# Kernel optimization log

Measured on AMD Instinct MI355X. Metric: run time of the kernel, lower is better.

Reference implementation:

```python
import jax, jax.numpy as jnp
import numpy as np
from jax import lax

THRESHOLD = 1.0
TAU_M = 10.0
TAU_S = 5.0
T_REF = 2.0


def setup_inputs() -> dict:
    key = jax.random.key(0)
    k1, k2, k3, k4 = jax.random.split(key, 4)
    T, B, I, O = 256, 128, 1024, 512
    x = (jax.random.uniform(k1, (T, B, I)) < 0.2).astype(jnp.float32)
    weight = jax.random.normal(k2, (O, I), dtype=jnp.float32) * 0.05
    bias = jax.random.normal(k3, (O,), dtype=jnp.float32) * 0.01
    weight_lateral = jax.random.normal(k4, (O,), dtype=jnp.float32) * 0.01
    return {"x": x, "weight": weight, "bias": bias, "weight_lateral": weight_lateral}


def reference(x, weight, bias, weight_lateral):
    # x: [T, B, I]; weight: [O, I]; bias, weight_lateral: [O]
    T, B, I = x.shape
    O = weight.shape[0]
    f32 = x.dtype
    decay_s = jnp.asarray(1.0 - 1.0 / TAU_S, f32)
    decay_m = jnp.asarray(1.0 - 1.0 / TAU_M, f32)

    def step(carry, xt):
        ep, u, o, v_ref, t_pre, t_post, t = carry
        # per-step linear + lateral feedback of previous output spikes
        i_resp = xt @ weight.T + bias + o * weight_lateral  # [B, O]
        ep = ep * decay_s + i_resp
        u = u * decay_m + ep / TAU_S
        u = u * (1.0 - (v_ref > 0).astype(f32))        # refractory gating
        o = (u > THRESHOLD).astype(f32)                # spike
        v_ref = jnp.clip(T_REF * o + (v_ref - 1.0), 0.0, T_REF)
        t_pre = jnp.maximum(xt * (t + 1.0) - 1.0, t_pre)   # last pre-spike time
        t_post = jnp.maximum(o * (t + 1.0) - 1.0, t_post)  # last post-spike time
        return (ep, u, o, v_ref, t_pre, t_post, t + 1.0), o

    zBO = jnp.zeros((B, O), f32)
    init = (zBO, zBO, zBO, zBO,
            jnp.full((B, I), -1.0, f32),
            jnp.full((B, O), -1.0, f32),
            jnp.asarray(0.0, f32))
    carry, output = lax.scan(step, init, x)
    times_pre, times_post = carry[4], carry[5]
    return output, times_pre, times_post
```

## Files before the change

kernel.cpp:

```cpp
#include <hip/hip_runtime.h>

#define T_STEPS 256
#define B_SZ 128
#define I_SZ 1024
#define O_SZ 512

typedef short bf16x8 __attribute__((ext_vector_type(8)));
typedef float f32x16 __attribute__((ext_vector_type(16)));

#define PLANE (O_SZ * I_SZ)
#define WS_NEEDED ((size_t)3 * PLANE * 2)

__device__ __forceinline__ ushort f2bf_rne(float f) {
    uint u = __float_as_uint(f);
    u += ((u >> 16) & 1u) + 0x7fffu;
    return (ushort)(u >> 16);
}
__device__ __forceinline__ uint pk2(float lo, float hi) {
    return (__float_as_uint(lo) >> 16) | (__float_as_uint(hi) & 0xffff0000u);
}
__device__ __forceinline__ void gload_lds16(const void* g, void* l) {
    typedef const void __attribute__((address_space(1))) gvt;
    typedef void __attribute__((address_space(3))) svt;
    __builtin_amdgcn_global_load_lds((gvt*)g, (svt*)l, 16, 0, 0);
}

__global__ __launch_bounds__(256) void wsplit_kernel(
    const float* __restrict__ W, ushort* __restrict__ wsp)
{
    const int t = blockIdx.x * 256 + threadIdx.x;
    const int n = t >> 7, kq = t & 127, k0 = kq * 8;
    const float* wp = W + (size_t)n * I_SZ + k0;

    uint q1[4], q2[4], q3[4];
#pragma unroll
    for (int jj = 0; jj < 4; ++jj) {
        ushort s1[2], s2[2], s3[2];
#pragma unroll
        for (int e = 0; e < 2; ++e) {
            float w0 = wp[jj * 2 + e];
            ushort a1 = f2bf_rne(w0);
            float  f1 = __uint_as_float((uint)a1 << 16);
            float  r1 = w0 - f1;
            ushort a2 = f2bf_rne(r1);
            float  f2 = __uint_as_float((uint)a2 << 16);
            float  r2 = r1 - f2;
            ushort a3 = f2bf_rne(r2);
            s1[e] = a1; s2[e] = a2; s3[e] = a3;
        }
        q1[jj] = (uint)s1[0] | ((uint)s1[1] << 16);
        q2[jj] = (uint)s2[0] | ((uint)s2[1] << 16);
        q3[jj] = (uint)s3[0] | ((uint)s3[1] << 16);
    }
    const int kt = k0 >> 5, k16 = (k0 >> 4) & 1, kh = (k0 >> 3) & 1;
    const int l = (n & 31) | (kh << 5), nsg = n >> 5;
    const size_t off = ((((size_t)kt * 16 + nsg) * 2 + k16) * 64 + l) * 8;
    *(uint4*)(wsp + off)             = make_uint4(q1[0], q1[1], q1[2], q1[3]);
    *(uint4*)(wsp + PLANE + off)     = make_uint4(q2[0], q2[1], q2[2], q2[3]);
    *(uint4*)(wsp + 2 * PLANE + off) = make_uint4(q3[0], q3[1], q3[2], q3[3]);
}

__global__ __launch_bounds__(512, 2) void gemm_mfma4(
    const float* __restrict__ X, const ushort* __restrict__ wsp,
    const float* __restrict__ bias, float* __restrict__ S)
{
    __shared__ uint ldsA[8192];
    __shared__ uint ldsB[24576];

    const int tid  = threadIdx.x;
    const int lane = tid & 63;
    const int w    = tid >> 6;
    const int wm   = w >> 2, wn = w & 3;

    const int bid     = blockIdx.x;
    const int logical = (bid & 7) * 32 + (bid >> 3);
    const int mb = logical >> 1, nb = logical & 1;
    const int row0 = mb * 256;

    const int arow = w * 32 + (lane >> 3);
    const int akq  = lane & 7;
    const float* pa = X + (size_t)(row0 + arow) * I_SZ + akq * 4;
    uint adst[4];
#pragma unroll
    for (int i = 0; i < 4; ++i) {
        const int row = arow + i * 8;
        adst[i] = (((row >> 5) * 2 + (akq >> 2)) * 64 +
                   ((row & 31) | (((akq >> 1) & 1) << 5))) * 4 + (akq & 1) * 2;
    }

    uint bsrc[6];
    const int c0 = w * 6;
#pragma unroll
    for (int i = 0; i < 6; ++i) {
        const int c = c0 + i, p = c >> 4, rr = (c >> 1) & 7, k16 = c & 1;
        bsrc[i] = (uint)p * PLANE + (uint)(((nb * 8 + rr) * 2 + k16) * 512) + lane * 8;
    }

    f32x16 acc[4][2];
#pragma unroll
    for (int i = 0; i < 4; ++i)
#pragma unroll
        for (int j = 0; j < 2; ++j)
#pragma unroll
            for (int r = 0; r < 16; ++r) acc[i][j][r] = 0.f;

#define BFRAG(BASE, P, SN, SS) \
    (*(const bf16x8*)((BASE) + (((P) * 8 + wn * 2 + (SN)) * 2 + (SS)) * 256 + lane * 4))

#define CLUSTER(B00, B01, B10, B11) do {                                      \
    __builtin_amdgcn_s_setprio(1);                                            \
    _Pragma("unroll")                                                         \
    for (int m_ = 0; m_ < 4; ++m_) {                                          \
        acc[m_][0] = __builtin_amdgcn_mfma_f32_32x32x16_bf16(af[m_][0], B00, acc[m_][0], 0, 0, 0); \
        acc[m_][0] = __builtin_amdgcn_mfma_f32_32x32x16_bf16(af[m_][1], B01, acc[m_][0], 0, 0, 0); \
        acc[m_][1] = __builtin_amdgcn_mfma_f32_32x32x16_bf16(af[m_][0], B10, acc[m_][1], 0, 0, 0); \
        acc[m_][1] = __builtin_amdgcn_mfma_f32_32x32x16_bf16(af[m_][1], B11, acc[m_][1], 0, 0, 0); \
    }                                                                         \
    __builtin_amdgcn_s_setprio(0);                                            \
} while (0)

    {
#pragma unroll
        for (int i = 0; i < 6; ++i)
            gload_lds16(wsp + bsrc[i], ldsB + (c0 + i) * 256);
        float4 a0 = *(const float4*)(pa);
        float4 a1 = *(const float4*)(pa + 8 * I_SZ);
        float4 a2 = *(const float4*)(pa + 16 * I_SZ);
        float4 a3 = *(const float4*)(pa + 24 * I_SZ);
        *(uint2*)(ldsA + adst[0]) = make_uint2(pk2(a0.x, a0.y), pk2(a0.z, a0.w));
        *(uint2*)(ldsA + adst[1]) = make_uint2(pk2(a1.x, a1.y), pk2(a1.z, a1.w));
        *(uint2*)(ldsA + adst[2]) = make_uint2(pk2(a2.x, a2.y), pk2(a2.z, a2.w));
        *(uint2*)(ldsA + adst[3]) = make_uint2(pk2(a3.x, a3.y), pk2(a3.z, a3.w));
        __syncthreads();
    }

    for (int kt = 0; kt < 32; ++kt) {
        const int cur = kt & 1;
        const uint* Ac = ldsA + cur * 4096;
        const uint* Bc = ldsB + cur * 12288;
        uint* An = ldsA + (cur ^ 1) * 4096;
        uint* Bn = ldsB + (cur ^ 1) * 12288;
        const bool pref = (kt < 31);

        float4 a0, a1, a2, a3;
        if (pref) {
            const uint kadd = (uint)(kt + 1) * 16384;
#pragma unroll
            for (int i = 0; i < 6; ++i)
                gload_lds16(wsp + bsrc[i] + kadd, Bn + (c0 + i) * 256);
            const float* p_ = pa + (kt + 1) * 32;
            a0 = *(const float4*)(p_);
            a1 = *(const float4*)(p_ + 8 * I_SZ);
            a2 = *(const float4*)(p_ + 16 * I_SZ);
            a3 = *(const float4*)(p_ + 24 * I_SZ);
        }

        bf16x8 af[4][2];
#pragma unroll
        for (int m = 0; m < 4; ++m)
#pragma unroll
            for (int s = 0; s < 2; ++s)
                af[m][s] = *(const bf16x8*)(Ac + (((wm * 4 + m) * 2 + s) * 64 + lane) * 4);

        bf16x8 c00 = BFRAG(Bc, 0, 0, 0), c01 = BFRAG(Bc, 0, 0, 1);
        bf16x8 c10 = BFRAG(Bc, 0, 1, 0), c11 = BFRAG(Bc, 0, 1, 1);
        bf16x8 n00 = BFRAG(Bc, 1, 0, 0), n01 = BFRAG(Bc, 1, 0, 1);
        bf16x8 n10 = BFRAG(Bc, 1, 1, 0), n11 = BFRAG(Bc, 1, 1, 1);
        CLUSTER(c00, c01, c10, c11);
        c00 = BFRAG(Bc, 2, 0, 0); c01 = BFRAG(Bc, 2, 0, 1);
        c10 = BFRAG(Bc, 2, 1, 0); c11 = BFRAG(Bc, 2, 1, 1);
        CLUSTER(n00, n01, n10, n11);
        CLUSTER(c00, c01, c10, c11);

        if (pref) {
            *(uint2*)(An + adst[0]) = make_uint2(pk2(a0.x, a0.y), pk2(a0.z, a0.w));
            *(uint2*)(An + adst[1]) = make_uint2(pk2(a1.x, a1.y), pk2(a1.z, a1.w));
            *(uint2*)(An + adst[2]) = make_uint2(pk2(a2.x, a2.y), pk2(a2.z, a2.w));
            *(uint2*)(An + adst[3]) = make_uint2(pk2(a3.x, a3.y), pk2(a3.z, a3.w));
        }
        __syncthreads();
    }

    const int colb = nb * 256 + wn * 64 + (lane & 31);
    const int rowbase = row0 + wm * 128 + 4 * (lane >> 5);
    float bv[2];
#pragma unroll
    for (int sn = 0; sn < 2; ++sn) bv[sn] = bias[colb + sn * 32];
#pragma unroll
    for (int m = 0; m < 4; ++m)
#pragma unroll
        for (int sn = 0; sn < 2; ++sn)
#pragma unroll
            for (int r = 0; r < 16; ++r) {
                const int rr = rowbase + m * 32 + (r & 3) + 8 * (r >> 2);
                S[(size_t)rr * O_SZ + colb + sn * 32] = acc[m][sn][r] + bv[sn];
            }
#undef BFRAG
#undef CLUSTER
}

#define BM 128
#define BN 128
#define BKF 32
#define LDT 132

__global__ __launch_bounds__(256, 2) void gemm_fp32(
    const float* __restrict__ X, const float* __restrict__ W,
    const float* __restrict__ bias, float* __restrict__ S)
{
    __shared__ float As[BKF][LDT];
    __shared__ float Ws[BKF][LDT];
    const int tid = threadIdx.x;
    const int nb = blockIdx.x & 3;
    const int mb = blockIdx.x >> 2;
    const int tx = (tid & 7) | ((tid & 128) >> 4);
    const int ty = (tid >> 3) & 15;
    const float* Ablk = X + (size_t)mb * BM * I_SZ;
    const float* Wblk = W + (size_t)nb * BN * I_SZ;
    const int skq = tid & 7;
    const int srow = tid >> 3;
    float acc[8][8];
#pragma unroll
    for (int i = 0; i < 8; ++i)
#pragma unroll
        for (int j = 0; j < 8; ++j) acc[i][j] = 0.f;
    for (int kt = 0; kt < I_SZ; kt += BKF) {
#pragma unroll
        for (int it = 0; it < 4; ++it) {
            const int row = srow + it * 32;
            float4 a = *(const float4*)(Ablk + (size_t)row * I_SZ + kt + skq * 4);
            As[skq * 4 + 0][row] = a.x; As[skq * 4 + 1][row] = a.y;
            As[skq * 4 + 2][row] = a.z; As[skq * 4 + 3][row] = a.w;
            float4 wv = *(const float4*)(Wblk + (size_t)row * I_SZ + kt + skq * 4);
            Ws[skq * 4 + 0][row] = wv.x; Ws[skq * 4 + 1][row] = wv.y;
            Ws[skq * 4 + 2][row] = wv.z; Ws[skq * 4 + 3][row] = wv.w;
        }
        __syncthreads();
#pragma unroll
        for (int kk = 0; kk < BKF; ++kk) {
            float4 a0 = *(const float4*)&As[kk][ty * 8];
            float4 a1 = *(const float4*)&As[kk][ty * 8 + 4];
            float4 w0 = *(const float4*)&Ws[kk][tx * 8];
            float4 w1 = *(const float4*)&Ws[kk][tx * 8 + 4];
            float av[8] = {a0.x, a0.y, a0.z, a0.w, a1.x, a1.y, a1.z, a1.w};
            float wv[8] = {w0.x, w0.y, w0.z, w0.w, w1.x, w1.y, w1.z, w1.w};
#pragma unroll
            for (int i = 0; i < 8; ++i)
#pragma unroll
                for (int j = 0; j < 8; ++j) acc[i][j] += av[i] * wv[j];
        }
        __syncthreads();
    }
    const int row0 = mb * BM + ty * 8;
    const int col0 = nb * BN + tx * 8;
    float bv[8];
#pragma unroll
    for (int j = 0; j < 8; ++j) bv[j] = bias[col0 + j];
#pragma unroll
    for (int i = 0; i < 8; ++i) {
        float4 o0 = {acc[i][0] + bv[0], acc[i][1] + bv[1], acc[i][2] + bv[2], acc[i][3] + bv[3]};
        float4 o1 = {acc[i][4] + bv[4], acc[i][5] + bv[5], acc[i][6] + bv[6], acc[i][7] + bv[7]};
        *(float4*)(S + (size_t)(row0 + i) * O_SZ + col0)     = o0;
        *(float4*)(S + (size_t)(row0 + i) * O_SZ + col0 + 4) = o1;
    }
}

__global__ __launch_bounds__(256) void scan_tpre_kernel(
    float* __restrict__ out, const float* __restrict__ wl_arr,
    const float* __restrict__ x)
{
    const int bid = blockIdx.x;
    if (bid < 256) {
#pragma clang fp contract(off)
        const int gid = bid * 256 + threadIdx.x;
        const float wl = wl_arr[gid & (O_SZ - 1)];
        const float decay_s = 0.8f;
        const float decay_m = 0.9f;

        float cur[8], nxt[8];
#pragma unroll
        for (int i = 0; i < 8; ++i) cur[i] = out[(size_t)i * (B_SZ * O_SZ) + gid];

        float ep = 0.f, u = 0.f, osp = 0.f, vref = 0.f, tpost = -1.f;
        for (int tb = 0; tb < T_STEPS; tb += 8) {
            if (tb < T_STEPS - 8) {
#pragma unroll
                for (int i = 0; i < 8; ++i)
                    nxt[i] = out[(size_t)(tb + 8 + i) * (B_SZ * O_SZ) + gid];
            }
#pragma unroll
            for (int i = 0; i < 8; ++i) {
                const int t = tb + i;
                const size_t idx = (size_t)t * (B_SZ * O_SZ) + gid;
                float iresp = cur[i] + osp * wl;
                ep = ep * decay_s + iresp;
                u  = u * decay_m + ep / 5.0f;
                if (vref > 0.f) u = 0.f;
                osp = (u > 1.0f) ? 1.f : 0.f;
                float v = 2.0f * osp + (vref - 1.0f);
                vref = v < 0.f ? 0.f : (v > 2.f ? 2.f : v);
                float cand = osp * ((float)t + 1.0f) - 1.0f;
                tpost = cand > tpost ? cand : tpost;
                out[idx] = osp;
            }
#pragma unroll
            for (int i = 0; i < 8; ++i) cur[i] = nxt[i];
        }
        out[(size_t)T_STEPS * B_SZ * O_SZ + (size_t)B_SZ * I_SZ + gid] = tpost;
    } else {
        const int gid = (bid - 256) * 256 + threadIdx.x;
        float tp = -1.f;
        for (int t = T_STEPS - 1; t >= 0; --t) {
            if (x[(size_t)t * (B_SZ * I_SZ) + gid] > 0.5f) { tp = (float)t; break; }
        }
        out[(size_t)T_STEPS * B_SZ * O_SZ + gid] = tp;
    }
}

extern "C" void kernel_launch(void* const* d_in, const int* in_sizes, int n_in,
                              void* d_out, int out_size, void* d_ws, size_t ws_size,
                              hipStream_t stream) {
    const float* x    = (const float*)d_in[0];
    const float* w    = (const float*)d_in[1];
    const float* bias = (const float*)d_in[2];
    const float* wl   = (const float*)d_in[3];
    float* out = (float*)d_out;

    if (ws_size >= WS_NEEDED) {
        ushort* wsp = (ushort*)d_ws;
        wsplit_kernel<<<dim3(256), dim3(256), 0, stream>>>(w, wsp);
        gemm_mfma4<<<dim3(256), dim3(512), 0, stream>>>(x, wsp, bias, out);
    } else {
        gemm_fp32<<<dim3(1024), dim3(256), 0, stream>>>(x, w, bias, out);
    }
    scan_tpre_kernel<<<dim3(768), dim3(256), 0, stream>>>(out, wl, x);
}
```

Before: 139.4 us.

## Restructure MFMA GEMM main loop into phased pipeline with explicit waitcnt barriers

Replaces the double-buffered GEMM loop with a hand-scheduled pipeline. Each k-tile is split into three phases, one per weight split plane, and each phase issues its own next-tile global-to-LDS loads, with explicit vmcnt/lgkmcnt waits, raw s_barrier and sched_barrier fences. The A-tile load mapping changes to two threads per row writing 16-byte chunks, and the LDS buffers are merged into one array. The aim is to overlap global loads with MFMA work more finely and cut full __syncthreads stalls, at the cost of fragile hand-counted wait counts that could race if miscounted.

```diff
diff --git a/kernel.cpp b/kernel.cpp
--- a/kernel.cpp
+++ b/kernel.cpp
@@ -60,12 +60,11 @@
     *(uint4*)(wsp + 2 * PLANE + off) = make_uint4(q3[0], q3[1], q3[2], q3[3]);
 }
 
-__global__ __launch_bounds__(512, 2) void gemm_mfma4(
+__global__ __launch_bounds__(512, 2) void gemm_mfma5(
     const float* __restrict__ X, const ushort* __restrict__ wsp,
     const float* __restrict__ bias, float* __restrict__ S)
 {
-    __shared__ uint ldsA[8192];
-    __shared__ uint ldsB[24576];
+    __shared__ uint lds[32768];
 
     const int tid  = threadIdx.x;
     const int lane = tid & 63;
@@ -77,24 +76,16 @@
     const int mb = logical >> 1, nb = logical & 1;
     const int row0 = mb * 256;
 
-    const int arow = w * 32 + (lane >> 3);
-    const int akq  = lane & 7;
-    const float* pa = X + (size_t)(row0 + arow) * I_SZ + akq * 4;
-    uint adst[4];
-#pragma unroll
-    for (int i = 0; i < 4; ++i) {
-        const int row = arow + i * 8;
-        adst[i] = (((row >> 5) * 2 + (akq >> 2)) * 64 +
-                   ((row & 31) | (((akq >> 1) & 1) << 5))) * 4 + (akq & 1) * 2;
-    }
-
-    uint bsrc[6];
-    const int c0 = w * 6;
-#pragma unroll
-    for (int i = 0; i < 6; ++i) {
-        const int c = c0 + i, p = c >> 4, rr = (c >> 1) & 7, k16 = c & 1;
-        bsrc[i] = (uint)p * PLANE + (uint)(((nb * 8 + rr) * 2 + k16) * 512) + lane * 8;
-    }
+    const int ar = tid >> 1, ah = tid & 1;
+    const float* pa = X + (size_t)(row0 + ar) * I_SZ + ah * 16;
+    const uint aw0 = (((uint)(ar >> 5) * 2 + ah) * 64 + (ar & 31)) * 4;
+
+    uint bsrc[3][2];
+#pragma unroll
+    for (int p = 0; p < 3; ++p)
+#pragma unroll
+        for (int q = 0; q < 2; ++q)
+            bsrc[p][q] = (uint)p * PLANE + (uint)(((nb * 8 + w) * 2 + q) * 512) + lane * 8;
 
     f32x16 acc[4][2];
 #pragma unroll
@@ -104,99 +95,144 @@
 #pragma unroll
             for (int r = 0; r < 16; ++r) acc[i][j][r] = 0.f;
 
-#define BFRAG(BASE, P, SN, SS) \
-    (*(const bf16x8*)((BASE) + (((P) * 8 + wn * 2 + (SN)) * 2 + (SS)) * 256 + lane * 4))
-
-#define CLUSTER(B00, B01, B10, B11) do {                                      \
+#define READ_B(BC, P) do {                                                    \
+    _Pragma("unroll")                                                         \
+    for (int sn_ = 0; sn_ < 2; ++sn_)                                         \
+        _Pragma("unroll")                                                     \
+        for (int k_ = 0; k_ < 2; ++k_)                                        \
+            bf[sn_][k_] = *(const bf16x8*)((BC) + ((P) * 16 +                 \
+                (wn * 2 + sn_) * 2 + k_) * 256 + lane * 4);                   \
+} while (0)
+
+#define MFMA16() do {                                                         \
     __builtin_amdgcn_s_setprio(1);                                            \
     _Pragma("unroll")                                                         \
-    for (int m_ = 0; m_ < 4; ++m_) {                                          \
-        acc[m_][0] = __builtin_amdgcn_mfma_f32_32x32x16_bf16(af[m_][0], B00, acc[m_][0], 0, 0, 0); \
-        acc[m_][0] = __builtin_amdgcn_mfma_f32_32x32x16_bf16(af[m_][1], B01, acc[m_][0], 0, 0, 0); \
-        acc[m_][1] = __builtin_amdgcn_mfma_f32_32x32x16_bf16(af[m_][0], B10, acc[m_][1], 0, 0, 0); \
-        acc[m_][1] = __builtin_amdgcn_mfma_f32_32x32x16_bf16(af[m_][1], B11, acc[m_][1], 0, 0, 0); \
-    }                                                                         \
+    for (int k_ = 0; k_ < 2; ++k_)                                            \
+        _Pragma("unroll")                                                     \
+        for (int m_ = 0; m_ < 4; ++m_)                                        \
+            _Pragma("unroll")                                                 \
+            for (int sn_ = 0; sn_ < 2; ++sn_)                                 \
+                acc[m_][sn_] = __builtin_amdgcn_mfma_f32_32x32x16_bf16(       \
+                    af[m_][k_], bf[sn_][k_], acc[m_][sn_], 0, 0, 0);          \
     __builtin_amdgcn_s_setprio(0);                                            \
 } while (0)
 
     {
 #pragma unroll
-        for (int i = 0; i < 6; ++i)
-            gload_lds16(wsp + bsrc[i], ldsB + (c0 + i) * 256);
-        float4 a0 = *(const float4*)(pa);
-        float4 a1 = *(const float4*)(pa + 8 * I_SZ);
-        float4 a2 = *(const float4*)(pa + 16 * I_SZ);
-        float4 a3 = *(const float4*)(pa + 24 * I_SZ);
-        *(uint2*)(ldsA + adst[0]) = make_uint2(pk2(a0.x, a0.y), pk2(a0.z, a0.w));
-        *(uint2*)(ldsA + adst[1]) = make_uint2(pk2(a1.x, a1.y), pk2(a1.z, a1.w));
-        *(uint2*)(ldsA + adst[2]) = make_uint2(pk2(a2.x, a2.y), pk2(a2.z, a2.w));
-        *(uint2*)(ldsA + adst[3]) = make_uint2(pk2(a3.x, a3.y), pk2(a3.z, a3.w));
-        __syncthreads();
-    }
-
-    for (int kt = 0; kt < 32; ++kt) {
-        const int cur = kt & 1;
-        const uint* Ac = ldsA + cur * 4096;
-        const uint* Bc = ldsB + cur * 12288;
-        uint* An = ldsA + (cur ^ 1) * 4096;
-        uint* Bn = ldsB + (cur ^ 1) * 12288;
-        const bool pref = (kt < 31);
-
-        float4 a0, a1, a2, a3;
-        if (pref) {
-            const uint kadd = (uint)(kt + 1) * 16384;
-#pragma unroll
-            for (int i = 0; i < 6; ++i)
-                gload_lds16(wsp + bsrc[i] + kadd, Bn + (c0 + i) * 256);
-            const float* p_ = pa + (kt + 1) * 32;
-            a0 = *(const float4*)(p_);
-            a1 = *(const float4*)(p_ + 8 * I_SZ);
-            a2 = *(const float4*)(p_ + 16 * I_SZ);
-            a3 = *(const float4*)(p_ + 24 * I_SZ);
-        }
-
-        bf16x8 af[4][2];
+        for (int p = 0; p < 3; ++p) {
+            gload_lds16(wsp + bsrc[p][0], lds + 4096 + (p * 16 + w * 2 + 0) * 256);
+            gload_lds16(wsp + bsrc[p][1], lds + 4096 + (p * 16 + w * 2 + 1) * 256);
+        }
+        float4 g0 = *(const float4*)(pa);
+        float4 g1 = *(const float4*)(pa + 4);
+        float4 g2 = *(const float4*)(pa + 8);
+        float4 g3 = *(const float4*)(pa + 12);
+        asm volatile("s_waitcnt vmcnt(0)" ::: "memory");
+        *(uint4*)(lds + aw0)       = make_uint4(pk2(g0.x, g0.y), pk2(g0.z, g0.w),
+                                                pk2(g1.x, g1.y), pk2(g1.z, g1.w));
+        *(uint4*)(lds + aw0 + 128) = make_uint4(pk2(g2.x, g2.y), pk2(g2.z, g2.w),
+                                                pk2(g3.x, g3.y), pk2(g3.z, g3.w));
+        asm volatile("s_waitcnt lgkmcnt(0)" ::: "memory");
+        __builtin_amdgcn_s_barrier();
+        __builtin_amdgcn_sched_barrier(0);
+    }
+
+    bf16x8 af[4][2], bf[2][2];
+
+    for (int kt = 0; kt < 31; ++kt) {
+        const uint* Ac = lds + (kt & 1) * 16384;
+        const uint* Bc = Ac + 4096;
+        uint* An = lds + ((kt & 1) ^ 1) * 16384;
+        uint* Bn = An + 4096;
+        const uint kadd = (uint)(kt + 1) * 16384;
+
+        asm volatile("s_waitcnt vmcnt(4)" ::: "memory");
+        __builtin_amdgcn_sched_barrier(0);
 #pragma unroll
         for (int m = 0; m < 4; ++m)
 #pragma unroll
-            for (int s = 0; s < 2; ++s)
-                af[m][s] = *(const bf16x8*)(Ac + (((wm * 4 + m) * 2 + s) * 64 + lane) * 4);
-
-        bf16x8 c00 = BFRAG(Bc, 0, 0, 0), c01 = BFRAG(Bc, 0, 0, 1);
-        bf16x8 c10 = BFRAG(Bc, 0, 1, 0), c11 = BFRAG(Bc, 0, 1, 1);
-        bf16x8 n00 = BFRAG(Bc, 1, 0, 0), n01 = BFRAG(Bc, 1, 0, 1);
-        bf16x8 n10 = BFRAG(Bc, 1, 1, 0), n11 = BFRAG(Bc, 1, 1, 1);
-        CLUSTER(c00, c01, c10, c11);
-        c00 = BFRAG(Bc, 2, 0, 0); c01 = BFRAG(Bc, 2, 0, 1);
-        c10 = BFRAG(Bc, 2, 1, 0); c11 = BFRAG(Bc, 2, 1, 1);
-        CLUSTER(n00, n01, n10, n11);
-        CLUSTER(c00, c01, c10, c11);
-
-        if (pref) {
-            *(uint2*)(An + adst[0]) = make_uint2(pk2(a0.x, a0.y), pk2(a0.z, a0.w));
-            *(uint2*)(An + adst[1]) = make_uint2(pk2(a1.x, a1.y), pk2(a1.z, a1.w));
-            *(uint2*)(An + adst[2]) = make_uint2(pk2(a2.x, a2.y), pk2(a2.z, a2.w));
-            *(uint2*)(An + adst[3]) = make_uint2(pk2(a3.x, a3.y), pk2(a3.z, a3.w));
-        }
-        __syncthreads();
-    }
-
-    const int colb = nb * 256 + wn * 64 + (lane & 31);
+            for (int k16 = 0; k16 < 2; ++k16)
+                af[m][k16] = *(const bf16x8*)(Ac + ((wm * 4 + m) * 2 + k16) * 256 + lane * 4);
+        READ_B(Bc, 0);
+        const float* pk = pa + (kt + 1) * 32;
+        float4 g0 = *(const float4*)(pk);
+        float4 g1 = *(const float4*)(pk + 4);
+        float4 g2 = *(const float4*)(pk + 8);
+        float4 g3 = *(const float4*)(pk + 12);
+        gload_lds16(wsp + bsrc[0][0] + kadd, Bn + (w * 2 + 0) * 256);
+        gload_lds16(wsp + bsrc[0][1] + kadd, Bn + (w * 2 + 1) * 256);
+        __builtin_amdgcn_s_barrier();
+        asm volatile("s_waitcnt lgkmcnt(0)" ::: "memory");
+        __builtin_amdgcn_sched_barrier(0);
+        MFMA16();
+        __builtin_amdgcn_s_barrier();
+
+        asm volatile("s_waitcnt vmcnt(8)" ::: "memory");
+        __builtin_amdgcn_sched_barrier(0);
+        READ_B(Bc, 1);
+        gload_lds16(wsp + bsrc[1][0] + kadd, Bn + (16 + w * 2 + 0) * 256);
+        gload_lds16(wsp + bsrc[1][1] + kadd, Bn + (16 + w * 2 + 1) * 256);
+        __builtin_amdgcn_s_barrier();
+        asm volatile("s_waitcnt lgkmcnt(0)" ::: "memory");
+        __builtin_amdgcn_sched_barrier(0);
+        MFMA16();
+        __builtin_amdgcn_s_barrier();
+
+        asm volatile("s_waitcnt vmcnt(8)" ::: "memory");
+        __builtin_amdgcn_sched_barrier(0);
+        READ_B(Bc, 2);
+        asm volatile("s_waitcnt vmcnt(4)" ::: "memory");
+        __builtin_amdgcn_sched_barrier(0);
+        *(uint4*)(An + aw0)       = make_uint4(pk2(g0.x, g0.y), pk2(g0.z, g0.w),
+                                               pk2(g1.x, g1.y), pk2(g1.z, g1.w));
+        *(uint4*)(An + aw0 + 128) = make_uint4(pk2(g2.x, g2.y), pk2(g2.z, g2.w),
+                                               pk2(g3.x, g3.y), pk2(g3.z, g3.w));
+        gload_lds16(wsp + bsrc[2][0] + kadd, Bn + (32 + w * 2 + 0) * 256);
+        gload_lds16(wsp + bsrc[2][1] + kadd, Bn + (32 + w * 2 + 1) * 256);
+        asm volatile("s_waitcnt lgkmcnt(0)" ::: "memory");
+        __builtin_amdgcn_s_barrier();
+        __builtin_amdgcn_sched_barrier(0);
+        MFMA16();
+        __builtin_amdgcn_s_barrier();
+    }
+
+    {
+        const uint* Ac = lds + 16384;
+        const uint* Bc = Ac + 4096;
+        asm volatile("s_waitcnt vmcnt(4)" ::: "memory");
+        __builtin_amdgcn_sched_barrier(0);
+#pragma unroll
+        for (int m = 0; m < 4; ++m)
+#pragma unroll
+            for (int k16 = 0; k16 < 2; ++k16)
+                af[m][k16] = *(const bf16x8*)(Ac + ((wm * 4 + m) * 2 + k16) * 256 + lane * 4);
+        READ_B(Bc, 0);
+        MFMA16();
+        asm volatile("s_waitcnt vmcnt(2)" ::: "memory");
+        __builtin_amdgcn_sched_barrier(0);
+        READ_B(Bc, 1);
+        MFMA16();
+        asm volatile("s_waitcnt vmcnt(0)" ::: "memory");
+        __builtin_amdgcn_sched_barrier(0);
+        READ_B(Bc, 2);
+        MFMA16();
+    }
+
     const int rowbase = row0 + wm * 128 + 4 * (lane >> 5);
-    float bv[2];
-#pragma unroll
-    for (int sn = 0; sn < 2; ++sn) bv[sn] = bias[colb + sn * 32];
-#pragma unroll
-    for (int m = 0; m < 4; ++m)
-#pragma unroll
-        for (int sn = 0; sn < 2; ++sn)
+#pragma unroll
+    for (int sn = 0; sn < 2; ++sn) {
+        const int colb = nb * 256 + (wn * 2 + sn) * 32 + (lane & 31);
+        const float bv = bias[colb];
+#pragma unroll
+        for (int m = 0; m < 4; ++m)
 #pragma unroll
             for (int r = 0; r < 16; ++r) {
                 const int rr = rowbase + m * 32 + (r & 3) + 8 * (r >> 2);
-                S[(size_t)rr * O_SZ + colb + sn * 32] = acc[m][sn][r] + bv[sn];
+                S[(size_t)rr * O_SZ + colb] = acc[m][sn][r] + bv;
             }
-#undef BFRAG
-#undef CLUSTER
+    }
+#undef READ_B
+#undef MFMA16
 }
 
 #define BM 128
@@ -329,7 +365,7 @@
     if (ws_size >= WS_NEEDED) {
         ushort* wsp = (ushort*)d_ws;
         wsplit_kernel<<<dim3(256), dim3(256), 0, stream>>>(w, wsp);
-        gemm_mfma4<<<dim3(256), dim3(512), 0, stream>>>(x, wsp, bias, out);
+        gemm_mfma5<<<dim3(256), dim3(512), 0, stream>>>(x, wsp, bias, out);
     } else {
         gemm_fp32<<<dim3(1024), dim3(256), 0, stream>>>(x, w, bias, out);
     }
```

Measured after the change: 148.7 us. 6.7% more time.
